# Optimization experiments

Hardware: AMD Instinct MI355X
Metric: run time of the kernel (lower is better)

The kernel has to match this reference:

```python
import jax, jax.numpy as jnp
import numpy as np

# LIF / substrate constants (from config: dt=1.0, tau_mem=20.0, threshold=0.02)
DT_OVER_TAU = 1.0 / 20.0
V_TH = 0.02
ORTHO_GAIN = 1.4


@jax.custom_vjp
def spike_fn(u):
    # Heaviside spike on (v - v_threshold); surrogate gradient in bwd (snnTorch-style fast sigmoid)
    return (u >= 0.0).astype(u.dtype)

def _spike_fwd(u):
    return spike_fn(u), u

def _spike_bwd(u, g):
    surr = 1.0 / (1.0 + 10.0 * jnp.abs(u)) ** 2
    return (g * surr,)

spike_fn.defvjp(_spike_fwd, _spike_bwd)


def lif_step(current):
    # Fresh state v0 = 0: v1 = v0 + (dt/tau) * (I - v0) = (dt/tau) * I
    v = DT_OVER_TAU * current
    return spike_fn(v - V_TH)


def setup_inputs() -> dict:
    key = jax.random.key(0)
    ks = jax.random.split(key, 7)
    B, N_IN, H, N_OUT = 256, 2048, 4096, 2048
    x = jax.random.uniform(ks[0], (B, N_IN), dtype=jnp.float32)
    s_in = (jax.random.uniform(ks[1], (B, N_IN)) < 0.1).astype(jnp.float32)
    s_h1 = (jax.random.uniform(ks[2], (B, H)) < 0.1).astype(jnp.float32)
    s_h2 = (jax.random.uniform(ks[3], (B, H)) < 0.1).astype(jnp.float32)
    # nn.Linear weights [out, in]; orthogonal-like scale: rows ~ gain-normalized
    W1 = jax.random.normal(ks[4], (H, N_IN), dtype=jnp.float32) * (ORTHO_GAIN / np.sqrt(N_IN))
    W2 = jax.random.normal(ks[5], (H, H), dtype=jnp.float32) * (ORTHO_GAIN / np.sqrt(H))
    W3 = jax.random.normal(ks[6], (N_OUT, H), dtype=jnp.float32) * (ORTHO_GAIN / np.sqrt(H))
    return {"x": x, "s_in": s_in, "s_h1": s_h1, "s_h2": s_h2, "W1": W1, "W2": W2, "W3": W3}


def reference(x, s_in, s_h1, s_h2, W1, W2, W3):
    # _integrate_inputs: gather prev spikes along topology edges, Linear, sum per target;
    # external input x goes to the 'input' group.
    cur_in = x                       # [B, N_IN]
    cur_h1 = s_in @ W1.T             # input  -> hidden1
    cur_h2 = s_h1 @ W2.T             # hidden1 -> hidden2
    cur_out = s_h2 @ W3.T            # hidden2 -> output
    # _update_neuron_dynamics: per-group LIF update + threshold
    sp_in = lif_step(cur_in)
    sp_h1 = lif_step(cur_h1)
    sp_h2 = lif_step(cur_h2)
    sp_out = lif_step(cur_out)
    # forward_step returns the dict of all group spikes; concatenate along features
    return jnp.concatenate([sp_in, sp_h1, sp_h2, sp_out], axis=-1)  # [B, 12288]
```

## Files before the change

kernel.cpp:

```cpp
#include <hip/hip_runtime.h>
#include <stdint.h>


typedef __attribute__((ext_vector_type(8))) short short8;
typedef __attribute__((ext_vector_type(4))) short short4v;
typedef __attribute__((ext_vector_type(4))) float f32x4;
typedef __attribute__((ext_vector_type(4))) unsigned int uint4v;

typedef __attribute__((address_space(1))) void gvoid;
typedef __attribute__((address_space(3))) void lvoid;

__device__ __forceinline__ void gload_lds16(const void* g, void* l) {
  __builtin_amdgcn_global_load_lds((gvoid*)g, (lvoid*)l, 16, 0, 0);
}

__device__ __forceinline__ unsigned short f2bf(float f) {
  unsigned u = __float_as_uint(f);
  return (unsigned short)((u + 0x7fffu + ((u >> 16) & 1u)) >> 16);
}

__device__ __forceinline__ float spike_of(float cur) {
  float v = __fmul_rn(cur, 0.05f);
  float u = __fsub_rn(v, 0.02f);
  return (u >= 0.0f) ? 1.0f : 0.0f;
}

__device__ __forceinline__ void split3(float w0, float w1,
                                       unsigned& hp, unsigned& mp, unsigned& lp) {
  unsigned u0 = __float_as_uint(w0), u1 = __float_as_uint(w1);
  unsigned hf0 = u0 & 0xFFFF0000u, hf1 = u1 & 0xFFFF0000u;
  hp = hf1 | (u0 >> 16);
  float r0 = w0 - __uint_as_float(hf0);
  float r1 = w1 - __uint_as_float(hf1);
  unsigned ru0 = __float_as_uint(r0), ru1 = __float_as_uint(r1);
  unsigned mf0 = ru0 & 0xFFFF0000u, mf1 = ru1 & 0xFFFF0000u;
  mp = mf1 | (ru0 >> 16);
  float q0 = r0 - __uint_as_float(mf0);
  float q1 = r1 - __uint_as_float(mf1);
  lp = (__float_as_uint(q1) & 0xFFFF0000u) | (__float_as_uint(q0) >> 16);
}

#define SB_IN_ELE   0
#define SB_H1_ELE   524288
#define SB_H2_ELE   1572864
#define PART_OFF_B  5242880
#define PART_STRIDE (256 * 6144)

__global__ __launch_bounds__(256) void prep_kernel(
    const float* __restrict__ x, const float* __restrict__ s_in,
    const float* __restrict__ s_h1, const float* __restrict__ s_h2,
    float* __restrict__ out, unsigned short* __restrict__ sb) {
  int e = blockIdx.x * 256 + threadIdx.x;
  if (e < 131072) {
    int f = e << 2;
    int b = f >> 11;
    int j = f & 2047;
    f32x4 v = *(const f32x4*)(x + f);
    f32x4 o;
    o.x = spike_of(v.x); o.y = spike_of(v.y);
    o.z = spike_of(v.z); o.w = spike_of(v.w);
    *(f32x4*)(out + (size_t)b * 12288 + j) = o;
  } else {
    const float* src;
    unsigned short* dst;
    int f;
    if (e < 262144)      { f = (e - 131072) << 2; src = s_in; dst = sb + SB_IN_ELE; }
    else if (e < 524288) { f = (e - 262144) << 2; src = s_h1; dst = sb + SB_H1_ELE; }
    else                 { f = (e - 524288) << 2; src = s_h2; dst = sb + SB_H2_ELE; }
    f32x4 v = *(const f32x4*)(src + f);
    short4v o = { (short)f2bf(v.x), (short)f2bf(v.y), (short)f2bf(v.z), (short)f2bf(v.w) };
    *(short4v*)(dst + f) = o;
  }
}

#define BK 64

__global__ __launch_bounds__(256, 2) void gemm_kernel(
    const unsigned short* __restrict__ sb, const float* __restrict__ W1,
    const float* __restrict__ W2, const float* __restrict__ W3,
    float* __restrict__ part, float* __restrict__ out) {
  __shared__ __align__(16) unsigned short As[256 * BK];
  __shared__ __align__(16) float Ws[32 * BK];

  const int blk = blockIdx.x;
  int g, nt, kp;
  if (blk < 256)      { g = 1; nt = blk & 127; kp = blk >> 7; }
  else if (blk < 384) { g = 0; nt = blk - 256; kp = 0; }
  else                { int l = blk - 384; g = 2; nt = l & 63; kp = l >> 6; }

  const int K = (g == 0) ? 2048 : 4096;
  const unsigned short* A = (g == 0) ? (sb + SB_IN_ELE)
                         : (g == 1) ? (sb + SB_H1_ELE) : (sb + SB_H2_ELE);
  const float* W = (g == 0) ? W1 : (g == 1) ? W2 : W3;

  const int n0 = nt * 32;
  const int k0 = kp * 2048;

  const int t    = threadIdx.x;
  const int lane = t & 63;
  const int w    = t >> 6;
  const int wm   = w * 64;
  const int l15  = lane & 15;
  const int lg   = lane >> 4;

  size_t a_src[8]; int a_dst[8];
#pragma unroll
  for (int i = 0; i < 8; i++) {
    int S = i * 256 + t;
    int r = S >> 3;
    int c = ((S & 7) ^ (r & 7)) << 3;
    a_src[i] = (size_t)r * K + c;
    a_dst[i] = S * 16;
  }
  size_t w_src[2]; int w_dst[2];
#pragma unroll
  for (int i = 0; i < 2; i++) {
    int S = i * 256 + t;
    int r = S >> 4;
    int c = ((S & 15) ^ (r & 15)) << 2;
    w_src[i] = (size_t)(n0 + r) * K + c;
    w_dst[i] = S * 16;
  }

  int a_rowb[4];
#pragma unroll
  for (int mi = 0; mi < 4; mi++) a_rowb[mi] = (wm + mi * 16 + l15) * 128;
  const int akey = l15 & 7;
  int w_rowb[2];
#pragma unroll
  for (int nf = 0; nf < 2; nf++) w_rowb[nf] = (nf * 16 + l15) * 256;

  f32x4 accH[4][2], accL[4][2];
#pragma unroll
  for (int i = 0; i < 4; i++)
#pragma unroll
    for (int j = 0; j < 2; j++) {
      accH[i][j] = (f32x4){0.f, 0.f, 0.f, 0.f};
      accL[i][j] = (f32x4){0.f, 0.f, 0.f, 0.f};
    }

  for (int s = 0; s < 32; s++) {
    const int kt = k0 + s * BK;

    __syncthreads();
#pragma unroll
    for (int i = 0; i < 8; i++)
      gload_lds16(A + a_src[i] + kt, (char*)As + a_dst[i]);
#pragma unroll
    for (int i = 0; i < 2; i++)
      gload_lds16(W + w_src[i] + kt, (char*)Ws + w_dst[i]);
    __syncthreads();

#pragma unroll
    for (int ks = 0; ks < 2; ks++) {
      const int aslot16 = ((ks * 4 + lg) ^ akey) * 16;
      short8 af[4];
#pragma unroll
      for (int mi = 0; mi < 4; mi++)
        af[mi] = *(const short8*)((const char*)As + a_rowb[mi] + aslot16);

      const int sA16 = (((ks * 8 + lg * 2)    ) ^ l15) * 16;
      const int sB16 = (((ks * 8 + lg * 2) + 1) ^ l15) * 16;
#pragma unroll
      for (int nf = 0; nf < 2; nf++) {
        f32x4 v0 = *(const f32x4*)((const char*)Ws + w_rowb[nf] + sA16);
        f32x4 v1 = *(const f32x4*)((const char*)Ws + w_rowb[nf] + sB16);
        unsigned h0, m0, q0, h1, m1, q1, h2, m2, q2, h3, m3, q3;
        split3(v0.x, v0.y, h0, m0, q0);
        split3(v0.z, v0.w, h1, m1, q1);
        split3(v1.x, v1.y, h2, m2, q2);
        split3(v1.z, v1.w, h3, m3, q3);
        uint4v hi  = {h0, h1, h2, h3};
        uint4v mid = {m0, m1, m2, m3};
        uint4v lo  = {q0, q1, q2, q3};
        short8 bh = __builtin_bit_cast(short8, hi);
        short8 bm = __builtin_bit_cast(short8, mid);
        short8 bl = __builtin_bit_cast(short8, lo);
#pragma unroll
        for (int mi = 0; mi < 4; mi++)
          accH[mi][nf] = __builtin_amdgcn_mfma_f32_16x16x32_bf16(af[mi], bh, accH[mi][nf], 0, 0, 0);
#pragma unroll
        for (int mi = 0; mi < 4; mi++)
          accL[mi][nf] = __builtin_amdgcn_mfma_f32_16x16x32_bf16(af[mi], bm, accL[mi][nf], 0, 0, 0);
#pragma unroll
        for (int mi = 0; mi < 4; mi++)
          accL[mi][nf] = __builtin_amdgcn_mfma_f32_16x16x32_bf16(af[mi], bl, accL[mi][nf], 0, 0, 0);
      }
    }
  }

  if (g == 0) {
#pragma unroll
    for (int mi = 0; mi < 4; mi++) {
      int row0 = wm + mi * 16 + (lg << 2);
#pragma unroll
      for (int nf = 0; nf < 2; nf++) {
        int col = 2048 + n0 + nf * 16 + l15;
#pragma unroll
        for (int r = 0; r < 4; r++)
          out[(size_t)(row0 + r) * 12288 + col] =
              spike_of(accH[mi][nf][r] + accL[mi][nf][r]);
      }
    }
  } else {
    const int colbase = (g == 1) ? 0 : 4096;
    float* pbase = part + (size_t)kp * PART_STRIDE;
#pragma unroll
    for (int mi = 0; mi < 4; mi++) {
      int row0 = wm + mi * 16 + (lg << 2);
#pragma unroll
      for (int nf = 0; nf < 2; nf++) {
        int col = colbase + n0 + nf * 16 + l15;
#pragma unroll
        for (int r = 0; r < 4; r++)
          pbase[(size_t)(row0 + r) * 6144 + col] = accH[mi][nf][r] + accL[mi][nf][r];
      }
    }
  }
}

__global__ __launch_bounds__(256) void reduce_kernel(
    const float* __restrict__ part, float* __restrict__ out) {
  int e = blockIdx.x * 256 + threadIdx.x;
  int f = e << 2;
  int b = f / 6144;
  int j = f - b * 6144;
  const float* p = part + (size_t)b * 6144 + j;
  f32x4 s0 = *(const f32x4*)(p);
  f32x4 s1 = *(const f32x4*)(p + (size_t)PART_STRIDE);
  f32x4 c = s0 + s1;
  f32x4 o;
  o.x = spike_of(c.x); o.y = spike_of(c.y);
  o.z = spike_of(c.z); o.w = spike_of(c.w);
  *(f32x4*)(out + (size_t)b * 12288 + 6144 + j) = o;
}

extern "C" void kernel_launch(void* const* d_in, const int* in_sizes, int n_in,
                              void* d_out, int out_size, void* d_ws, size_t ws_size,
                              hipStream_t stream) {
  const float* x    = (const float*)d_in[0];
  const float* s_in = (const float*)d_in[1];
  const float* s_h1 = (const float*)d_in[2];
  const float* s_h2 = (const float*)d_in[3];
  const float* W1   = (const float*)d_in[4];
  const float* W2   = (const float*)d_in[5];
  const float* W3   = (const float*)d_in[6];
  float* out = (float*)d_out;

  unsigned short* sb = (unsigned short*)d_ws;
  float* part = (float*)((char*)d_ws + PART_OFF_B);

  prep_kernel<<<3072, 256, 0, stream>>>(x, s_in, s_h1, s_h2, out, sb);
  gemm_kernel<<<512, 256, 0, stream>>>(sb, W1, W2, W3, part, out);
  reduce_kernel<<<1536, 256, 0, stream>>>(part, out);
}
```

Measured before the change: 203.2 us.

## Double-buffer LDS and widen GEMM tile to 64 columns with 512 threads

Moves the GEMM to 512-thread blocks, each computing a 256x64 output tile with a 2x4 wave layout, which halves the block count and reuses each staged A tile across twice as many columns. It adds double-buffered LDS staging so the next K-step's global-to-LDS loads run while the current step computes, synchronised with explicit vmcnt waits and barriers. LDS use rises to 96KB per block, and with only 256 blocks occupancy and load balance across CUs may fall.

```diff
diff --git a/kernel.cpp b/kernel.cpp
--- a/kernel.cpp
+++ b/kernel.cpp
@@ -74,39 +74,40 @@
 }
 
 #define BK 64
-
-__global__ __launch_bounds__(256, 2) void gemm_kernel(
+#define LDS_W_BASE 65536
+
+__global__ __launch_bounds__(512, 2) void gemm_kernel(
     const unsigned short* __restrict__ sb, const float* __restrict__ W1,
     const float* __restrict__ W2, const float* __restrict__ W3,
     float* __restrict__ part, float* __restrict__ out) {
-  __shared__ __align__(16) unsigned short As[256 * BK];
-  __shared__ __align__(16) float Ws[32 * BK];
+  __shared__ __align__(16) char lds[98304];
 
   const int blk = blockIdx.x;
   int g, nt, kp;
-  if (blk < 256)      { g = 1; nt = blk & 127; kp = blk >> 7; }
-  else if (blk < 384) { g = 0; nt = blk - 256; kp = 0; }
-  else                { int l = blk - 384; g = 2; nt = l & 63; kp = l >> 6; }
+  if (blk < 128)      { g = 1; nt = blk & 63; kp = blk >> 6; }
+  else if (blk < 192) { g = 0; nt = blk - 128; kp = 0; }
+  else                { int l = blk - 192; g = 2; nt = l & 31; kp = l >> 5; }
 
   const int K = (g == 0) ? 2048 : 4096;
   const unsigned short* A = (g == 0) ? (sb + SB_IN_ELE)
                          : (g == 1) ? (sb + SB_H1_ELE) : (sb + SB_H2_ELE);
   const float* W = (g == 0) ? W1 : (g == 1) ? W2 : W3;
 
-  const int n0 = nt * 32;
+  const int n0 = nt * 64;
   const int k0 = kp * 2048;
 
   const int t    = threadIdx.x;
   const int lane = t & 63;
   const int w    = t >> 6;
-  const int wm   = w * 64;
+  const int wm   = (w >> 1) * 64;
+  const int wn   = (w & 1) * 32;
   const int l15  = lane & 15;
   const int lg   = lane >> 4;
 
-  size_t a_src[8]; int a_dst[8];
-#pragma unroll
-  for (int i = 0; i < 8; i++) {
-    int S = i * 256 + t;
+  size_t a_src[4]; int a_dst[4];
+#pragma unroll
+  for (int i = 0; i < 4; i++) {
+    int S = i * 512 + t;
     int r = S >> 3;
     int c = ((S & 7) ^ (r & 7)) << 3;
     a_src[i] = (size_t)r * K + c;
@@ -115,7 +116,7 @@
   size_t w_src[2]; int w_dst[2];
 #pragma unroll
   for (int i = 0; i < 2; i++) {
-    int S = i * 256 + t;
+    int S = i * 512 + t;
     int r = S >> 4;
     int c = ((S & 15) ^ (r & 15)) << 2;
     w_src[i] = (size_t)(n0 + r) * K + c;
@@ -128,7 +129,7 @@
   const int akey = l15 & 7;
   int w_rowb[2];
 #pragma unroll
-  for (int nf = 0; nf < 2; nf++) w_rowb[nf] = (nf * 16 + l15) * 256;
+  for (int nf = 0; nf < 2; nf++) w_rowb[nf] = (wn + nf * 16 + l15) * 256;
 
   f32x4 accH[4][2], accL[4][2];
 #pragma unroll
@@ -139,32 +140,34 @@
       accL[i][j] = (f32x4){0.f, 0.f, 0.f, 0.f};
     }
 
-  for (int s = 0; s < 32; s++) {
-    const int kt = k0 + s * BK;
-
-    __syncthreads();
-#pragma unroll
-    for (int i = 0; i < 8; i++)
-      gload_lds16(A + a_src[i] + kt, (char*)As + a_dst[i]);
+  auto stage = [&](int buf, int kt) {
+    const int aoff = buf << 15;
+    const int woff = LDS_W_BASE + (buf << 14);
+#pragma unroll
+    for (int i = 0; i < 4; i++)
+      gload_lds16(A + a_src[i] + kt, lds + aoff + a_dst[i]);
 #pragma unroll
     for (int i = 0; i < 2; i++)
-      gload_lds16(W + w_src[i] + kt, (char*)Ws + w_dst[i]);
-    __syncthreads();
-
+      gload_lds16(W + w_src[i] + kt, lds + woff + w_dst[i]);
+  };
+
+  auto compute = [&](int buf) {
+    const char* pA = lds + (buf << 15);
+    const char* pW = lds + LDS_W_BASE + (buf << 14);
 #pragma unroll
     for (int ks = 0; ks < 2; ks++) {
       const int aslot16 = ((ks * 4 + lg) ^ akey) * 16;
       short8 af[4];
 #pragma unroll
       for (int mi = 0; mi < 4; mi++)
-        af[mi] = *(const short8*)((const char*)As + a_rowb[mi] + aslot16);
+        af[mi] = *(const short8*)(pA + a_rowb[mi] + aslot16);
 
       const int sA16 = (((ks * 8 + lg * 2)    ) ^ l15) * 16;
       const int sB16 = (((ks * 8 + lg * 2) + 1) ^ l15) * 16;
 #pragma unroll
       for (int nf = 0; nf < 2; nf++) {
-        f32x4 v0 = *(const f32x4*)((const char*)Ws + w_rowb[nf] + sA16);
-        f32x4 v1 = *(const f32x4*)((const char*)Ws + w_rowb[nf] + sB16);
+        f32x4 v0 = *(const f32x4*)(pW + w_rowb[nf] + sA16);
+        f32x4 v1 = *(const f32x4*)(pW + w_rowb[nf] + sB16);
         unsigned h0, m0, q0, h1, m1, q1, h2, m2, q2, h3, m3, q3;
         split3(v0.x, v0.y, h0, m0, q0);
         split3(v0.z, v0.w, h1, m1, q1);
@@ -187,6 +190,23 @@
           accL[mi][nf] = __builtin_amdgcn_mfma_f32_16x16x32_bf16(af[mi], bl, accL[mi][nf], 0, 0, 0);
       }
     }
+  };
+
+  stage(0, k0);
+  for (int s = 0; s < 32; s++) {
+    const int cur = s & 1;
+    if (s < 31) {
+      stage(cur ^ 1, k0 + (s + 1) * BK);
+      asm volatile("s_waitcnt vmcnt(6)" ::: "memory");
+    } else {
+      asm volatile("s_waitcnt vmcnt(0)" ::: "memory");
+    }
+    __builtin_amdgcn_s_barrier();
+    __builtin_amdgcn_sched_barrier(0);
+    compute(cur);
+    asm volatile("s_waitcnt lgkmcnt(0)" ::: "memory");
+    __builtin_amdgcn_s_barrier();
+    __builtin_amdgcn_sched_barrier(0);
   }
 
   if (g == 0) {
@@ -195,7 +215,7 @@
       int row0 = wm + mi * 16 + (lg << 2);
 #pragma unroll
       for (int nf = 0; nf < 2; nf++) {
-        int col = 2048 + n0 + nf * 16 + l15;
+        int col = 2048 + n0 + wn + nf * 16 + l15;
 #pragma unroll
         for (int r = 0; r < 4; r++)
           out[(size_t)(row0 + r) * 12288 + col] =
@@ -210,7 +230,7 @@
       int row0 = wm + mi * 16 + (lg << 2);
 #pragma unroll
       for (int nf = 0; nf < 2; nf++) {
-        int col = colbase + n0 + nf * 16 + l15;
+        int col = colbase + n0 + wn + nf * 16 + l15;
 #pragma unroll
         for (int r = 0; r < 4; r++)
           pbase[(size_t)(row0 + r) * 6144 + col] = accH[mi][nf][r] + accL[mi][nf][r];
@@ -251,6 +271,6 @@
   float* part = (float*)((char*)d_ws + PART_OFF_B);
 
   prep_kernel<<<3072, 256, 0, stream>>>(x, s_in, s_h1, s_h2, out, sb);
-  gemm_kernel<<<512, 256, 0, stream>>>(sb, W1, W2, W3, part, out);
+  gemm_kernel<<<256, 512, 0, stream>>>(sb, W1, W2, W3, part, out);
   reduce_kernel<<<1536, 256, 0, stream>>>(part, out);
 }
```

Result: faster. 189.7 us (-6.7%).
